# Kernel optimization log

Hardware: AMD Instinct MI355X
Metric: run time of the kernel (lower is better)

Reference implementation:

```python
import jax, jax.numpy as jnp
import numpy as np

DEGREE = 8
START_DEGREE = 0


def setup_inputs() -> dict:
    key = jax.random.key(0)
    k1, k2 = jax.random.split(key)
    B, IN, OUT = 4096, 1024, 1024
    width = DEGREE - START_DEGREE + 1  # 9
    x = jax.random.normal(k1, (B, IN), dtype=jnp.float32)
    coeffs = jax.random.normal(k2, (OUT, width), dtype=jnp.float32) * 0.1
    input_scale = jnp.ones((1,), dtype=jnp.float32)
    return {"x": x, "coeffs": coeffs, "input_scale": input_scale}


def reference(x, coeffs, input_scale):
    # scale + squash input to [-1, 1] (Legendre domain)
    scale = jnp.clip(input_scale, 0.1, 2.0)
    xs = jnp.tanh(x * scale)  # [B, I]

    # Bonnet recursion: P0 = 1, P1 = x, Pn = ((2n-1) x P_{n-1} - (n-1) P_{n-2}) / n
    polys = [jnp.ones_like(xs)]
    if DEGREE >= 1:
        polys.append(xs)
        for n in range(2, DEGREE + 1):
            Pn = ((2 * n - 1) * xs * polys[-1] - (n - 1) * polys[-2]) / n
            polys.append(jnp.clip(Pn, -100.0, 100.0))

    P = jnp.stack(polys[START_DEGREE:DEGREE + 1], axis=1)  # [B, W, I]
    # original: (P[:,None] * coeffs[None,:,:,None]).sum(2).sum(-1) == einsum
    return jnp.einsum("bwi,ow->bo", P, coeffs)  # [B, O]
```

## Files before the change

### kernel.cpp

```cpp
#include <hip/hip_runtime.h>


constexpr int I_DIM = 1024;
constexpr int O_DIM = 1024;
constexpr int NT    = 256;
constexpr int G     = 4;

__global__ __launch_bounds__(NT, 4) void legendre_fused(
    const float* __restrict__ x,
    const float* __restrict__ coeffs,
    const float* __restrict__ scale_p,
    float* __restrict__ out)
{
    __shared__ float S_lds[G][8];

    const int t    = threadIdx.x;
    const int wave = t >> 6;
    const int lane = t & 63;
    const int b0   = blockIdx.x * G;
    const int row  = b0 + wave;

    float sc = fminf(fmaxf(scale_p[0], 0.1f), 2.0f);
    const float K = sc * 2.8853900817779268f;

    float c[36];
    {
        const float4* ct4 = reinterpret_cast<const float4*>(coeffs) + (size_t)t * 9;
        #pragma unroll
        for (int k = 0; k < 9; ++k) {
            float4 v = ct4[k];
            c[4 * k + 0] = v.x; c[4 * k + 1] = v.y;
            c[4 * k + 2] = v.z; c[4 * k + 3] = v.w;
        }
    }

    const float4* xr = reinterpret_cast<const float4*>(x + (size_t)row * I_DIM) + lane;
    float4 xv[4];
    #pragma unroll
    for (int k = 0; k < 4; ++k) xv[k] = xr[k * 64];

    const float An[7] = {1.5f, 5.f/3.f, 1.75f, 1.8f, 11.f/6.f, 13.f/7.f, 1.875f};
    const float Bn[7] = {0.5f, 2.f/3.f, 0.75f, 0.8f, 5.f/6.f,  6.f/7.f,  0.875f};

    float s[8] = {0.f, 0.f, 0.f, 0.f, 0.f, 0.f, 0.f, 0.f};
    #pragma unroll
    for (int k = 0; k < 4; ++k) {
        const float vals[4] = {xv[k].x, xv[k].y, xv[k].z, xv[k].w};
        #pragma unroll
        for (int e = 0; e < 4; ++e) {
            float ex = __builtin_amdgcn_exp2f(vals[e] * K);
            float xs = 1.f - 2.f * __builtin_amdgcn_rcpf(ex + 1.f);
            float pm2 = 1.f, pm1 = xs;
            s[0] += xs;
            #pragma unroll
            for (int n = 0; n < 7; ++n) {
                float pn = An[n] * xs * pm1 - Bn[n] * pm2;
                s[n + 1] += pn;
                pm2 = pm1; pm1 = pn;
            }
        }
    }

    #pragma unroll
    for (int w = 0; w < 8; ++w) {
        float v = s[w];
        #pragma unroll
        for (int m = 32; m >= 1; m >>= 1)
            v += __shfl_xor(v, m, 64);
        if (lane == 0) S_lds[wave][w] = v;
    }
    __syncthreads();

    #pragma unroll
    for (int r = 0; r < G; ++r) {
        float s0 = S_lds[r][0], s1 = S_lds[r][1], s2 = S_lds[r][2], s3 = S_lds[r][3];
        float s4 = S_lds[r][4], s5 = S_lds[r][5], s6 = S_lds[r][6], s7 = S_lds[r][7];

        float4 acc;
        float* ap = &acc.x;
        #pragma unroll
        for (int ol = 0; ol < 4; ++ol) {
            float a = c[ol * 9 + 0] * (float)I_DIM;
            a = fmaf(c[ol * 9 + 1], s0, a);
            a = fmaf(c[ol * 9 + 2], s1, a);
            a = fmaf(c[ol * 9 + 3], s2, a);
            a = fmaf(c[ol * 9 + 4], s3, a);
            a = fmaf(c[ol * 9 + 5], s4, a);
            a = fmaf(c[ol * 9 + 6], s5, a);
            a = fmaf(c[ol * 9 + 7], s6, a);
            a = fmaf(c[ol * 9 + 8], s7, a);
            ap[ol] = a;
        }
        *reinterpret_cast<float4*>(out + (size_t)(b0 + r) * O_DIM + 4 * t) = acc;
    }
}

extern "C" void kernel_launch(void* const* d_in, const int* in_sizes, int n_in,
                              void* d_out, int out_size, void* d_ws, size_t ws_size,
                              hipStream_t stream) {
    const float* x      = (const float*)d_in[0];
    const float* coeffs = (const float*)d_in[1];
    const float* scale  = (const float*)d_in[2];
    float* out          = (float*)d_out;

    const int B = in_sizes[0] / I_DIM;
    const int nblocks = B / G;

    legendre_fused<<<nblocks, NT, 0, stream>>>(x, coeffs, scale, out);
}
```

Before: 14.50 us.

## Replace per-element Bonnet recursion with power-sum moments and closed-form Legendre conversion

Each lane now accumulates raw power sums xs^1..xs^8 instead of running the Legendre recursion per element. After the wave reduction, lane 0 turns the summed moments into summed Legendre values using fixed monomial coefficients. The x and coeff loads are issued earlier so they overlap with the scale setup, and output stores become nontemporal. The power basis can lose precision through cancellation at degree 8, and the per-degree clip to ±100 is dropped, though it cannot trigger for inputs in [-1,1].

```diff
diff --git a/kernel.cpp b/kernel.cpp
--- a/kernel.cpp
+++ b/kernel.cpp
@@ -5,6 +5,8 @@
 constexpr int O_DIM = 1024;
 constexpr int NT    = 256;
 constexpr int G     = 4;
+
+typedef float f32x4 __attribute__((ext_vector_type(4)));
 
 __global__ __launch_bounds__(NT, 4) void legendre_fused(
     const float* __restrict__ x,
@@ -20,64 +22,81 @@
     const int b0   = blockIdx.x * G;
     const int row  = b0 + wave;
 
+    const float4* xr = reinterpret_cast<const float4*>(x + (size_t)row * I_DIM) + lane;
+    float4 xv0 = xr[0];
+    float4 xv1 = xr[64];
+    float4 xv2 = xr[128];
+    float4 xv3 = xr[192];
+
+    const float4* ct4 = reinterpret_cast<const float4*>(coeffs) + (size_t)t * 9;
+    float4 cv[9];
+    #pragma unroll
+    for (int k = 0; k < 9; ++k) cv[k] = ct4[k];
+
     float sc = fminf(fmaxf(scale_p[0], 0.1f), 2.0f);
     const float K = sc * 2.8853900817779268f;
 
-    float c[36];
-    {
-        const float4* ct4 = reinterpret_cast<const float4*>(coeffs) + (size_t)t * 9;
-        #pragma unroll
-        for (int k = 0; k < 9; ++k) {
-            float4 v = ct4[k];
-            c[4 * k + 0] = v.x; c[4 * k + 1] = v.y;
-            c[4 * k + 2] = v.z; c[4 * k + 3] = v.w;
-        }
+    float m1 = 0.f, m2 = 0.f, m3 = 0.f, m4 = 0.f,
+          m5 = 0.f, m6 = 0.f, m7 = 0.f, m8 = 0.f;
+
+    const float vals[16] = {xv0.x, xv0.y, xv0.z, xv0.w,
+                            xv1.x, xv1.y, xv1.z, xv1.w,
+                            xv2.x, xv2.y, xv2.z, xv2.w,
+                            xv3.x, xv3.y, xv3.z, xv3.w};
+    #pragma unroll
+    for (int e = 0; e < 16; ++e) {
+        float ex = __builtin_amdgcn_exp2f(vals[e] * K);
+        float xs = fmaf(-2.f, __builtin_amdgcn_rcpf(ex + 1.f), 1.f);
+        float p2 = xs * xs;
+        float p3 = p2 * xs;
+        float p4 = p2 * p2;
+        m1 += xs;
+        m2 += p2;
+        m3 += p3;
+        m4 += p4;
+        m5 = fmaf(p2, p3, m5);
+        m6 = fmaf(p3, p3, m6);
+        m7 = fmaf(p3, p4, m7);
+        m8 = fmaf(p4, p4, m8);
     }
 
-    const float4* xr = reinterpret_cast<const float4*>(x + (size_t)row * I_DIM) + lane;
-    float4 xv[4];
+    float mm[8] = {m1, m2, m3, m4, m5, m6, m7, m8};
     #pragma unroll
-    for (int k = 0; k < 4; ++k) xv[k] = xr[k * 64];
-
-    const float An[7] = {1.5f, 5.f/3.f, 1.75f, 1.8f, 11.f/6.f, 13.f/7.f, 1.875f};
-    const float Bn[7] = {0.5f, 2.f/3.f, 0.75f, 0.8f, 5.f/6.f,  6.f/7.f,  0.875f};
-
-    float s[8] = {0.f, 0.f, 0.f, 0.f, 0.f, 0.f, 0.f, 0.f};
-    #pragma unroll
-    for (int k = 0; k < 4; ++k) {
-        const float vals[4] = {xv[k].x, xv[k].y, xv[k].z, xv[k].w};
+    for (int w = 0; w < 8; ++w) {
         #pragma unroll
-        for (int e = 0; e < 4; ++e) {
-            float ex = __builtin_amdgcn_exp2f(vals[e] * K);
-            float xs = 1.f - 2.f * __builtin_amdgcn_rcpf(ex + 1.f);
-            float pm2 = 1.f, pm1 = xs;
-            s[0] += xs;
-            #pragma unroll
-            for (int n = 0; n < 7; ++n) {
-                float pn = An[n] * xs * pm1 - Bn[n] * pm2;
-                s[n + 1] += pn;
-                pm2 = pm1; pm1 = pn;
-            }
-        }
+        for (int msk = 32; msk >= 1; msk >>= 1)
+            mm[w] += __shfl_xor(mm[w], msk, 64);
     }
 
-    #pragma unroll
-    for (int w = 0; w < 8; ++w) {
-        float v = s[w];
-        #pragma unroll
-        for (int m = 32; m >= 1; m >>= 1)
-            v += __shfl_xor(v, m, 64);
-        if (lane == 0) S_lds[wave][w] = v;
+    if (lane == 0) {
+        const float M1 = mm[0], M2 = mm[1], M3 = mm[2], M4 = mm[3],
+                    M5 = mm[4], M6 = mm[5], M7 = mm[6], M8 = mm[7];
+        const float N = (float)I_DIM;
+        S_lds[wave][0] = M1;
+        S_lds[wave][1] = 1.5f * M2 - 0.5f * N;
+        S_lds[wave][2] = 2.5f * M3 - 1.5f * M1;
+        S_lds[wave][3] = 4.375f * M4 - 3.75f * M2 + 0.375f * N;
+        S_lds[wave][4] = 7.875f * M5 - 8.75f * M3 + 1.875f * M1;
+        S_lds[wave][5] = 14.4375f * M6 - 19.6875f * M4 + 6.5625f * M2 - 0.3125f * N;
+        S_lds[wave][6] = 26.8125f * M7 - 43.3125f * M5 + 19.6875f * M3 - 2.1875f * M1;
+        S_lds[wave][7] = 50.2734375f * M8 - 93.84375f * M6 + 54.140625f * M4
+                       - 9.84375f * M2 + 0.2734375f * N;
     }
     __syncthreads();
+
+    float c[36];
+    #pragma unroll
+    for (int k = 0; k < 9; ++k) {
+        c[4 * k + 0] = cv[k].x; c[4 * k + 1] = cv[k].y;
+        c[4 * k + 2] = cv[k].z; c[4 * k + 3] = cv[k].w;
+    }
 
     #pragma unroll
     for (int r = 0; r < G; ++r) {
         float s0 = S_lds[r][0], s1 = S_lds[r][1], s2 = S_lds[r][2], s3 = S_lds[r][3];
         float s4 = S_lds[r][4], s5 = S_lds[r][5], s6 = S_lds[r][6], s7 = S_lds[r][7];
 
-        float4 acc;
-        float* ap = &acc.x;
+        f32x4 acc;
         #pragma unroll
         for (int ol = 0; ol < 4; ++ol) {
             float a = c[ol * 9 + 0] * (float)I_DIM;
@@ -89,9 +108,10 @@
             a = fmaf(c[ol * 9 + 6], s5, a);
             a = fmaf(c[ol * 9 + 7], s6, a);
             a = fmaf(c[ol * 9 + 8], s7, a);
-            ap[ol] = a;
+            acc[ol] = a;
         }
-        *reinterpret_cast<float4*>(out + (size_t)(b0 + r) * O_DIM + 4 * t) = acc;
+        __builtin_nontemporal_store(acc,
+            reinterpret_cast<f32x4*>(out + (size_t)(b0 + r) * O_DIM + 4 * t));
     }
 }
 
```

After: 11.90 us (median of 2 runs). -17.9%, faster.
